# Performance work log

Measured on AMD Instinct MI355X. Metric: run time of the kernel, lower is better.

## Reference

```python
import jax, jax.numpy as jnp
import numpy as np

RADIUS = 12
SIGMA = 5.0
USM_LO, USM_HI = 0.0, 5.0
BEGIN = 0  # cfg.usm_begin_param


def _gauss_kernel_2d():
    x = jnp.arange(-RADIUS, RADIUS + 1, dtype=jnp.float32)
    k = jnp.exp(-0.5 * (x / SIGMA) ** 2)
    k = k / k.sum()
    return jnp.outer(k, k)  # [25, 25]


def setup_inputs() -> dict:
    key = jax.random.key(0)
    k1, k2 = jax.random.split(key)
    img = jax.random.uniform(k1, (16, 3, 512, 512), dtype=jnp.float32)
    features = jax.random.normal(k2, (16, 8), dtype=jnp.float32)
    return {"img": img, "features": features}


def reference(img, features):
    p = features[:, BEGIN:BEGIN + 1]                       # [B, 1]
    param = (jnp.tanh(p) * 0.5 + 0.5) * (USM_HI - USM_LO) + USM_LO

    # depthwise 25x25 gaussian blur with reflect padding
    kernel = jnp.broadcast_to(_gauss_kernel_2d(), (3, 1, 25, 25))  # OIHW, groups=3
    padded = jnp.pad(img, ((0, 0), (0, 0), (RADIUS, RADIUS), (RADIUS, RADIUS)),
                     mode='reflect')
    blurred = jax.lax.conv_general_dilated(
        padded, kernel, window_strides=(1, 1), padding='VALID',
        dimension_numbers=('NCHW', 'OIHW', 'NCHW'), feature_group_count=3)

    out = img + param.reshape(-1, 1, 1, 1) * (img - blurred)
    return out, param
```

## Files before the change

### kernel.cpp

```cpp
#include <hip/hip_runtime.h>
#include <hip/hip_fp16.h>


#define RADIUS 12
#define KS     25
#define TILE   64
#define PT     (TILE + 2 * RADIUS)
#define TA_LD  104
#define TB_LD  72
#define IMG_W  512
#define IMG_H  512
#define PLANE  (IMG_W * IMG_H)
#define NPLANE 48

#define N_STAGE (PT * 11)
#define N_H     (PT * (TILE / 8))

__device__ __constant__ float GW[KS] = {
    0.00453456f, 0.00718308f, 0.01093238f, 0.01598625f, 0.02245983f,
    0.03031760f, 0.03931982f, 0.04899550f, 0.05865827f, 0.06747307f,
    0.07456928f, 0.07918039f, 0.08077993f, 0.07918039f, 0.07456928f,
    0.06747307f, 0.05865827f, 0.04899550f, 0.03931982f, 0.03031760f,
    0.02245983f, 0.01598625f, 0.01093238f, 0.00718308f, 0.00453456f
};

__device__ __forceinline__ int reflect512(int i) {
    i = (i < 0) ? -i : i;
    return (i >= 512) ? (1022 - i) : i;
}

typedef _Float16 h2_t __attribute__((ext_vector_type(2)));

__device__ __forceinline__ unsigned h2u(__half2 h) {
    union { __half2 h; unsigned u; } x; x.h = h; return x.u;
}
__device__ __forceinline__ __half2 u2h(unsigned u) {
    union { unsigned u; __half2 h; } x; x.u = u; return x.h;
}
__device__ __forceinline__ float u_lo(unsigned u) {
    return __half2float(__low2half(u2h(u)));
}
__device__ __forceinline__ float u_hi(unsigned u) {
    return __half2float(__high2half(u2h(u)));
}

#if __has_builtin(__builtin_amdgcn_fdot2)
__device__ __forceinline__ float fdot2u(unsigned a, unsigned b, float c) {
    union { unsigned u; h2_t h; } ua, ub;
    ua.u = a; ub.u = b;
    return __builtin_amdgcn_fdot2(ua.h, ub.h, c, false);
}
#else
__device__ __forceinline__ float fdot2u(unsigned a, unsigned b, float c) {
    return c + u_lo(a) * u_lo(b) + u_hi(a) * u_hi(b);
}
#endif

__global__ __launch_bounds__(256) void usm_fused_kernel(
    const float* __restrict__ img, const float* __restrict__ feat,
    float* __restrict__ out, float* __restrict__ out_param)
{
    __shared__ __half tileA[PT][TA_LD];
    __shared__ __half tmpB[PT][TB_LD];

    const int bid  = blockIdx.x + 8 * blockIdx.y + 64 * blockIdx.z;
    const int swz  = (bid & 7) * 384 + (bid >> 3);
    const int bx   = swz & 7;
    const int by   = (swz >> 3) & 7;
    const int zc   = swz >> 6;

    const int tid = threadIdx.x;
    const int tx0 = bx * TILE, ty0 = by * TILE;
    const int b   = zc / 3;
    const float param = (tanhf(feat[b * 8]) * 0.5f + 0.5f) * 5.0f;
    const float* __restrict__ src = img + (size_t)zc * PLANE;
    const bool xedge = (bx == 0) || (bx == 7);

    unsigned W2[12];
#pragma unroll
    for (int m = 0; m < 12; ++m)
        W2[m] = h2u(__floats2half2_rn(GW[2 * m], GW[2 * m + 1]));
    const unsigned WE = h2u(__floats2half2_rn(GW[24], 0.f));
    const unsigned WO = h2u(__floats2half2_rn(0.f, GW[24]));

    __half2 GWh2[KS];
#pragma unroll
    for (int k = 0; k < KS; ++k)
        GWh2[k] = __floats2half2_rn(GW[k], GW[k]);

#pragma unroll
    for (int it = 0; it < 4; ++it) {
        const int li = tid + it * 256;
        if (it < 3 || li < N_STAGE) {
            const int py = li / 11, s = li - py * 11;
            const int gy = reflect512(ty0 - RADIUS + py);
            const float* __restrict__ rowp = src + (size_t)gy * IMG_W;
            const int gx = tx0 - RADIUS + s * 8;
            float4 va, vb;
            if (!xedge) {
                va = *(const float4*)(rowp + gx);
                vb = *(const float4*)(rowp + gx + 4);
            } else {
                va.x = rowp[reflect512(gx)];     va.y = rowp[reflect512(gx + 1)];
                va.z = rowp[reflect512(gx + 2)]; va.w = rowp[reflect512(gx + 3)];
                vb.x = rowp[reflect512(gx + 4)]; vb.y = rowp[reflect512(gx + 5)];
                vb.z = rowp[reflect512(gx + 6)]; vb.w = rowp[reflect512(gx + 7)];
            }
            uint4 pk;
            pk.x = h2u(__floats2half2_rn(va.x, va.y));
            pk.y = h2u(__floats2half2_rn(va.z, va.w));
            pk.z = h2u(__floats2half2_rn(vb.x, vb.y));
            pk.w = h2u(__floats2half2_rn(vb.z, vb.w));
            *(uint4*)&tileA[py][s * 8] = pk;
        }
    }
    __syncthreads();

#pragma unroll
    for (int it = 0; it < 3; ++it) {
        const int li = tid + it * 256;
        if (it < 2 || li < N_H) {
            const int py = li >> 3, g = li & 7;
            const uint4 qa = *(const uint4*)&tileA[py][g * 8];
            const uint4 qb = *(const uint4*)&tileA[py][g * 8 + 8];
            const uint4 qc = *(const uint4*)&tileA[py][g * 8 + 16];
            const uint4 qd = *(const uint4*)&tileA[py][g * 8 + 24];

            unsigned P[16] = { qa.x, qa.y, qa.z, qa.w, qb.x, qb.y, qb.z, qb.w,
                               qc.x, qc.y, qc.z, qc.w, qd.x, qd.y, qd.z, qd.w };
            unsigned S[15];
#pragma unroll
            for (int i = 0; i < 15; ++i)
                S[i] = __builtin_amdgcn_alignbit(P[i + 1], P[i], 16);

            float acc[8];
#pragma unroll
            for (int h = 0; h < 4; ++h) {
                float a = 0.f;
#pragma unroll
                for (int m = 0; m < 12; ++m) a = fdot2u(P[h + m], W2[m], a);
                acc[2 * h] = fdot2u(P[h + 12], WE, a);
            }
#pragma unroll
            for (int h = 0; h < 4; ++h) {
                float a = 0.f;
#pragma unroll
                for (int m = 0; m < 12; ++m) a = fdot2u(S[h + m], W2[m], a);
                acc[2 * h + 1] = fdot2u(P[h + 12], WO, a);
            }

            uint4 pk;
            pk.x = h2u(__floats2half2_rn(acc[0], acc[1]));
            pk.y = h2u(__floats2half2_rn(acc[2], acc[3]));
            pk.z = h2u(__floats2half2_rn(acc[4], acc[5]));
            pk.w = h2u(__floats2half2_rn(acc[6], acc[7]));
            *(uint4*)&tmpB[py][g * 8] = pk;
        }
    }
    __syncthreads();

    const int tx4 = (tid & 15) * 4, ry0 = (tid >> 4) * 4;

    __half2 aP0[4], aP1[4];
#pragma unroll
    for (int d = 0; d < 4; ++d) { aP0[d] = __half2(0, 0); aP1[d] = __half2(0, 0); }

#pragma unroll
    for (int k = 0; k < KS + 3; ++k) {
        const uint2 rd = *(const uint2*)&tmpB[ry0 + k][tx4];
        const __half2 p0 = u2h(rd.x), p1 = u2h(rd.y);
#pragma unroll
        for (int d = 0; d < 4; ++d) {
            const int kk = k - d;
            if (kk >= 0 && kk < KS) {
                aP0[d] = __hfma2(GWh2[kk], p0, aP0[d]);
                aP1[d] = __hfma2(GWh2[kk], p1, aP1[d]);
            }
        }
    }

    float* __restrict__ dst = out + (size_t)zc * PLANE;
#pragma unroll
    for (int d = 0; d < 4; ++d) {
        const int oy = ty0 + ry0 + d;
        const uint2 cv = *(const uint2*)&tileA[ry0 + d + RADIUS][tx4 + RADIUS];
        const float v0 = u_lo(cv.x), v1 = u_hi(cv.x), v2 = u_lo(cv.y), v3 = u_hi(cv.y);
        const float b0 = __half2float(__low2half(aP0[d])), b1 = __half2float(__high2half(aP0[d]));
        const float b2 = __half2float(__low2half(aP1[d])), b3 = __half2float(__high2half(aP1[d]));
        float4 o;
        o.x = v0 + param * (v0 - b0);
        o.y = v1 + param * (v1 - b1);
        o.z = v2 + param * (v2 - b2);
        o.w = v3 + param * (v3 - b3);
        *(float4*)(dst + (size_t)oy * IMG_W + tx0 + tx4) = o;
    }

    if (tid == 0 && bx == 0 && by == 0 && (zc - b * 3) == 0)
        out_param[b] = param;
}

extern "C" void kernel_launch(void* const* d_in, const int* in_sizes, int n_in,
                              void* d_out, int out_size, void* d_ws, size_t ws_size,
                              hipStream_t stream) {
    const float* img  = (const float*)d_in[0];
    const float* feat = (const float*)d_in[1];
    float* out       = (float*)d_out;
    float* out_param = (float*)d_out + (size_t)NPLANE * PLANE;

    usm_fused_kernel<<<dim3(8, 8, NPLANE), 256, 0, stream>>>(img, feat, out, out_param);
}
```

Before: 40.44 us.

## Compute horizontal blur pass with MFMA banded-matrix multiplies

Replaces the per-thread fdot2 horizontal 25-tap convolution with MFMA 16x16x32 f16 instructions. Each wave multiplies 16x64 input strips by a banded Toeplitz weight matrix built in registers. The LDS arrays are merged into one buffer, and the intermediate gets padded rows (96) because MFMA tiles cover 16-row groups past the 88-row halo. This offloads the arithmetic to the matrix cores, at the cost of wasted zero-weight work and scattered 2-byte LDS stores.

```diff
diff --git a/kernel.cpp b/kernel.cpp
--- a/kernel.cpp
+++ b/kernel.cpp
@@ -5,16 +5,17 @@
 #define RADIUS 12
 #define KS     25
 #define TILE   64
-#define PT     (TILE + 2 * RADIUS)
+#define PT     88
 #define TA_LD  104
 #define TB_LD  72
+#define TB_ROWS 96
 #define IMG_W  512
 #define IMG_H  512
 #define PLANE  (IMG_W * IMG_H)
 #define NPLANE 48
 
 #define N_STAGE (PT * 11)
-#define N_H     (PT * (TILE / 8))
+#define LDS_HALVES (PT * TA_LD + TB_ROWS * TB_LD)
 
 __device__ __constant__ float GW[KS] = {
     0.00453456f, 0.00718308f, 0.01093238f, 0.01598625f, 0.02245983f,
@@ -29,7 +30,8 @@
     return (i >= 512) ? (1022 - i) : i;
 }
 
-typedef _Float16 h2_t __attribute__((ext_vector_type(2)));
+typedef _Float16 f16x8 __attribute__((ext_vector_type(8)));
+typedef float f32x4 __attribute__((ext_vector_type(4)));
 
 __device__ __forceinline__ unsigned h2u(__half2 h) {
     union { __half2 h; unsigned u; } x; x.h = h; return x.u;
@@ -44,24 +46,13 @@
     return __half2float(__high2half(u2h(u)));
 }
 
-#if __has_builtin(__builtin_amdgcn_fdot2)
-__device__ __forceinline__ float fdot2u(unsigned a, unsigned b, float c) {
-    union { unsigned u; h2_t h; } ua, ub;
-    ua.u = a; ub.u = b;
-    return __builtin_amdgcn_fdot2(ua.h, ub.h, c, false);
-}
-#else
-__device__ __forceinline__ float fdot2u(unsigned a, unsigned b, float c) {
-    return c + u_lo(a) * u_lo(b) + u_hi(a) * u_hi(b);
-}
-#endif
-
 __global__ __launch_bounds__(256) void usm_fused_kernel(
     const float* __restrict__ img, const float* __restrict__ feat,
     float* __restrict__ out, float* __restrict__ out_param)
 {
-    __shared__ __half tileA[PT][TA_LD];
-    __shared__ __half tmpB[PT][TB_LD];
+    __shared__ __align__(16) __half lds[LDS_HALVES];
+#define TA(r, c) lds[(r) * TA_LD + (c)]
+#define TB(r, c) lds[PT * TA_LD + (r) * TB_LD + (c)]
 
     const int bid  = blockIdx.x + 8 * blockIdx.y + 64 * blockIdx.z;
     const int swz  = (bid & 7) * 384 + (bid >> 3);
@@ -76,12 +67,18 @@
     const float* __restrict__ src = img + (size_t)zc * PLANE;
     const bool xedge = (bx == 0) || (bx == 7);
 
-    unsigned W2[12];
+    const int lane = tid & 63, wid = tid >> 6;
+    const int r16 = lane & 15, kg = lane >> 4;
+
+    f16x8 B1, B2;
 #pragma unroll
-    for (int m = 0; m < 12; ++m)
-        W2[m] = h2u(__floats2half2_rn(GW[2 * m], GW[2 * m + 1]));
-    const unsigned WE = h2u(__floats2half2_rn(GW[24], 0.f));
-    const unsigned WO = h2u(__floats2half2_rn(0.f, GW[24]));
+    for (int i = 0; i < 8; ++i) {
+        const int k = kg * 8 + i;
+        const int d1 = k - r16;
+        B1[i] = (d1 >= 0 && d1 < KS) ? (_Float16)GW[d1] : (_Float16)0.f;
+        const int d2 = 32 + k - r16;
+        B2[i] = (d2 < KS) ? (_Float16)GW[d2] : (_Float16)0.f;
+    }
 
     __half2 GWh2[KS];
 #pragma unroll
@@ -111,51 +108,23 @@
             pk.y = h2u(__floats2half2_rn(va.z, va.w));
             pk.z = h2u(__floats2half2_rn(vb.x, vb.y));
             pk.w = h2u(__floats2half2_rn(vb.z, vb.w));
-            *(uint4*)&tileA[py][s * 8] = pk;
+            *(uint4*)&TA(py, s * 8) = pk;
         }
     }
     __syncthreads();
 
 #pragma unroll
-    for (int it = 0; it < 3; ++it) {
-        const int li = tid + it * 256;
-        if (it < 2 || li < N_H) {
-            const int py = li >> 3, g = li & 7;
-            const uint4 qa = *(const uint4*)&tileA[py][g * 8];
-            const uint4 qb = *(const uint4*)&tileA[py][g * 8 + 8];
-            const uint4 qc = *(const uint4*)&tileA[py][g * 8 + 16];
-            const uint4 qd = *(const uint4*)&tileA[py][g * 8 + 24];
-
-            unsigned P[16] = { qa.x, qa.y, qa.z, qa.w, qb.x, qb.y, qb.z, qb.w,
-                               qc.x, qc.y, qc.z, qc.w, qd.x, qd.y, qd.z, qd.w };
-            unsigned S[15];
+    for (int t = wid; t < 24; t += 4) {
+        const int py0 = (t >> 2) * 16;
+        const int c0  = (t & 3) * 16;
+        const f16x8 A1 = *(const f16x8*)&TA(py0 + r16, c0 + kg * 8);
+        const f16x8 A2 = *(const f16x8*)&TA(py0 + r16, c0 + 32);
+        f32x4 d = {0.f, 0.f, 0.f, 0.f};
+        d = __builtin_amdgcn_mfma_f32_16x16x32_f16(A2, B2, d, 0, 0, 0);
+        d = __builtin_amdgcn_mfma_f32_16x16x32_f16(A1, B1, d, 0, 0, 0);
 #pragma unroll
-            for (int i = 0; i < 15; ++i)
-                S[i] = __builtin_amdgcn_alignbit(P[i + 1], P[i], 16);
-
-            float acc[8];
-#pragma unroll
-            for (int h = 0; h < 4; ++h) {
-                float a = 0.f;
-#pragma unroll
-                for (int m = 0; m < 12; ++m) a = fdot2u(P[h + m], W2[m], a);
-                acc[2 * h] = fdot2u(P[h + 12], WE, a);
-            }
-#pragma unroll
-            for (int h = 0; h < 4; ++h) {
-                float a = 0.f;
-#pragma unroll
-                for (int m = 0; m < 12; ++m) a = fdot2u(S[h + m], W2[m], a);
-                acc[2 * h + 1] = fdot2u(P[h + 12], WO, a);
-            }
-
-            uint4 pk;
-            pk.x = h2u(__floats2half2_rn(acc[0], acc[1]));
-            pk.y = h2u(__floats2half2_rn(acc[2], acc[3]));
-            pk.z = h2u(__floats2half2_rn(acc[4], acc[5]));
-            pk.w = h2u(__floats2half2_rn(acc[6], acc[7]));
-            *(uint4*)&tmpB[py][g * 8] = pk;
-        }
+        for (int reg = 0; reg < 4; ++reg)
+            TB(py0 + kg * 4 + reg, c0 + r16) = __float2half(d[reg]);
     }
     __syncthreads();
 
@@ -167,7 +136,7 @@
 
 #pragma unroll
     for (int k = 0; k < KS + 3; ++k) {
-        const uint2 rd = *(const uint2*)&tmpB[ry0 + k][tx4];
+        const uint2 rd = *(const uint2*)&TB(ry0 + k, tx4);
         const __half2 p0 = u2h(rd.x), p1 = u2h(rd.y);
 #pragma unroll
         for (int d = 0; d < 4; ++d) {
@@ -183,7 +152,7 @@
 #pragma unroll
     for (int d = 0; d < 4; ++d) {
         const int oy = ty0 + ry0 + d;
-        const uint2 cv = *(const uint2*)&tileA[ry0 + d + RADIUS][tx4 + RADIUS];
+        const uint2 cv = *(const uint2*)&TA(ry0 + d + RADIUS, tx4 + RADIUS);
         const float v0 = u_lo(cv.x), v1 = u_hi(cv.x), v2 = u_lo(cv.y), v3 = u_hi(cv.y);
         const float b0 = __half2float(__low2half(aP0[d])), b1 = __half2float(__high2half(aP0[d]));
         const float b2 = __half2float(__low2half(aP1[d])), b3 = __half2float(__high2half(aP1[d]));
@@ -197,6 +166,8 @@
 
     if (tid == 0 && bx == 0 && by == 0 && (zc - b * 3) == 0)
         out_param[b] = param;
+#undef TA
+#undef TB
 }
 
 extern "C" void kernel_launch(void* const* d_in, const int* in_sizes, int n_in,
```

After: 44.48 us. 1.1x slower.
